# Optimization experiments

Hardware: AMD Instinct MI355X
Metric: run time of the kernel (lower is better)

## Reference

```python
import jax, jax.numpy as jnp
import numpy as np

B, S, E, H = 2, 2048, 768, 12
HD = E // H
EPS = 1e-5


def setup_inputs() -> dict:
    key = jax.random.key(0)
    ks = jax.random.split(key, 7)
    sc_in = 1.0 / np.sqrt(E)
    return {
        "x": jax.random.normal(ks[0], (B, S, E), dtype=jnp.float32),
        "gamma": jnp.ones((E,), dtype=jnp.float32),
        "beta": jnp.zeros((E,), dtype=jnp.float32),
        "Wqkv": jax.random.normal(ks[1], (3 * E, E), dtype=jnp.float32) * sc_in,
        "bqkv": jax.random.normal(ks[2], (3 * E,), dtype=jnp.float32) * 0.01,
        "Wo": jax.random.normal(ks[3], (E, E), dtype=jnp.float32) * sc_in,
        "bo": jax.random.normal(ks[4], (E,), dtype=jnp.float32) * 0.01,
    }


def reference(x, gamma, beta, Wqkv, bqkv, Wo, bo):
    # LayerNorm
    mu = jnp.mean(x, axis=-1, keepdims=True)
    var = jnp.mean(jnp.square(x - mu), axis=-1, keepdims=True)
    xn = (x - mu) * jax.lax.rsqrt(var + EPS) * gamma + beta
    # fused QKV projection; original reshapes to [B,S,H,3*hd] then chunks,
    # i.e. per-head blocks of 3*hd split into q/k/v slices of hd each.
    qkv = (xn @ Wqkv.T + bqkv).reshape(B, S, H, 3, HD)
    q, k, v = qkv[..., 0, :], qkv[..., 1, :], qkv[..., 2, :]  # [B,S,H,hd]
    scores = jnp.einsum("bshd,bthd->bhst", q, k) / np.sqrt(HD)
    attn = jax.nn.softmax(scores, axis=-1)  # [B,H,S,S]
    out = jnp.einsum("bhst,bthd->bshd", attn, v).reshape(B, S, E)
    return out @ Wo.T + bo
```

## Files before the change

kernel.cpp:

```cpp
#include <hip/hip_runtime.h>
#include <math.h>

#define B_  2
#define S_  2048
#define E_  768
#define H_  12
#define HD_ 64
#define M_  (B_ * S_)
#define N3E (3 * E_)

typedef __attribute__((ext_vector_type(8)))  short short8;
typedef __attribute__((ext_vector_type(4)))  short short4v;
typedef __attribute__((ext_vector_type(8)))  _Float16 half8;
typedef __attribute__((ext_vector_type(4)))  _Float16 half4;
typedef __attribute__((ext_vector_type(2)))  _Float16 half2_t;
typedef __attribute__((ext_vector_type(4)))  float floatx4;
typedef __attribute__((ext_vector_type(16))) float floatx16;

#define QSCALE 0.18033688011112042f

__device__ inline unsigned short f2bf(float f) {
  union { float f; unsigned u; } a; a.f = f;
  unsigned r = a.u + 0x7fff + ((a.u >> 16) & 1);
  return (unsigned short)(r >> 16);
}
__device__ inline unsigned short f2bf_fast(float f) {
  union { float f; unsigned u; } a; a.f = f;
  return (unsigned short)((a.u + 0x8000u) >> 16);
}
__device__ inline half2_t pkrtz(float a, float b) {
  return __builtin_bit_cast(half2_t, __builtin_amdgcn_cvt_pkrtz(a, b));
}

__global__ __launch_bounds__(256) void cvt2_kernel(
    const float* __restrict__ w1, const float* __restrict__ w2,
    unsigned short* __restrict__ d1, unsigned short* __restrict__ d2,
    int n1_4, int ntot4) {
  int i = blockIdx.x * 256 + threadIdx.x;
  if (i >= ntot4) return;
  const float* src; unsigned short* dst; int k;
  if (i < n1_4) { src = w1; dst = d1; k = i; }
  else          { src = w2; dst = d2; k = i - n1_4; }
  float4 f = *(const float4*)&src[k * 4];
  ushort4 r;
  r.x = f2bf(f.x); r.y = f2bf(f.y); r.z = f2bf(f.z); r.w = f2bf(f.w);
  *(ushort4*)&dst[k * 4] = r;
}

__global__ __launch_bounds__(256) void ln_kernel(
    const float* __restrict__ x, const float* __restrict__ gamma,
    const float* __restrict__ beta, unsigned short* __restrict__ xnb) {
  const int wv = threadIdx.x >> 6, lane = threadIdx.x & 63;
  const int row = blockIdx.x * 4 + wv;
  const float* xr = x + (size_t)row * E_;

  float4 a = ((const float4*)xr)[lane];
  float4 b = ((const float4*)xr)[lane + 64];
  float4 c = ((const float4*)xr)[lane + 128];

  float s  = (a.x + a.y) + (a.z + a.w) + (b.x + b.y) + (b.z + b.w)
           + (c.x + c.y) + (c.z + c.w);
  float s2 = a.x*a.x + a.y*a.y + a.z*a.z + a.w*a.w
           + b.x*b.x + b.y*b.y + b.z*b.z + b.w*b.w
           + c.x*c.x + c.y*c.y + c.z*c.z + c.w*c.w;
#pragma unroll
  for (int o = 32; o > 0; o >>= 1) {
    s  += __shfl_xor(s, o);
    s2 += __shfl_xor(s2, o);
  }
  const float mu  = s * (1.0f / E_);
  const float var = s2 * (1.0f / E_) - mu * mu;
  const float rs  = rsqrtf(var + 1e-5f);

  const float4* gp = (const float4*)gamma;
  const float4* bp = (const float4*)beta;
  ushort4* xo = (ushort4*)(xnb + (size_t)row * E_);

  float4 vin[3] = {a, b, c};
#pragma unroll
  for (int j = 0; j < 3; j++) {
    float4 g = gp[lane + 64 * j];
    float4 be = bp[lane + 64 * j];
    float4 v = vin[j];
    ushort4 r;
    r.x = f2bf((v.x - mu) * rs * g.x + be.x);
    r.y = f2bf((v.y - mu) * rs * g.y + be.y);
    r.z = f2bf((v.z - mu) * rs * g.z + be.z);
    r.w = f2bf((v.w - mu) * rs * g.w + be.w);
    xo[lane + 64 * j] = r;
  }
}

__global__ __launch_bounds__(256) void bgemm_kernel(
    const unsigned short* __restrict__ A, const unsigned short* __restrict__ Wb,
    const float* __restrict__ bias, int mode,
    unsigned short* __restrict__ qbf, unsigned short* __restrict__ kbf,
    _Float16* __restrict__ vth, float* __restrict__ out) {
  __shared__ __align__(16) unsigned short As[128 * 64];
  __shared__ __align__(16) unsigned short Bs[64 * 64];

  const int t  = threadIdx.x;
  const int ln = t & 63, wv = t >> 6;
  const int lr = ln & 15, lg = ln >> 4;
  const int m0 = blockIdx.x * 128, n0 = blockIdx.y * 64;
  const int w  = (mode == 1) ? 3 : ((n0 >> 6) % 3);

  const int srow = ln >> 3;
  const int scol = (ln & 7) * 8;

  const unsigned short* Ag = A  + (size_t)(m0 + wv * 32 + srow) * 768 + scol;
  const unsigned short* Bg = Wb + (size_t)(n0 + wv * 16 + srow) * 768 + scol;

  floatx4 acc[2][4];
#pragma unroll
  for (int i = 0; i < 2; i++)
#pragma unroll
    for (int j = 0; j < 4; j++) acc[i][j] = (floatx4){0.f, 0.f, 0.f, 0.f};

  for (int k0 = 0; k0 < 768; k0 += 64) {
    __syncthreads();
#pragma unroll
    for (int j = 0; j < 4; j++)
      __builtin_amdgcn_global_load_lds(
          (const __attribute__((address_space(1))) void*)(Ag + k0 + j * 8 * 768),
          (__attribute__((address_space(3))) void*)(&As[(wv * 32 + j * 8) * 64]),
          16, 0, 0);
#pragma unroll
    for (int j = 0; j < 2; j++)
      __builtin_amdgcn_global_load_lds(
          (const __attribute__((address_space(1))) void*)(Bg + k0 + j * 8 * 768),
          (__attribute__((address_space(3))) void*)(&Bs[(wv * 16 + j * 8) * 64]),
          16, 0, 0);
    __syncthreads();

#pragma unroll
    for (int kk = 0; kk < 2; kk++) {
      short8 af[2], bf[4];
#pragma unroll
      for (int i = 0; i < 2; i++)
        af[i] = *(const short8*)&As[(wv * 32 + i * 16 + lr) * 64 + kk * 32 + lg * 8];
#pragma unroll
      for (int j = 0; j < 4; j++)
        bf[j] = *(const short8*)&Bs[(j * 16 + lr) * 64 + kk * 32 + lg * 8];
      if (w < 2) {
#pragma unroll
        for (int i = 0; i < 2; i++)
#pragma unroll
          for (int j = 0; j < 4; j++)
            acc[i][j] = __builtin_amdgcn_mfma_f32_16x16x32_bf16(bf[j], af[i], acc[i][j], 0, 0, 0);
      } else {
#pragma unroll
        for (int i = 0; i < 2; i++)
#pragma unroll
          for (int j = 0; j < 4; j++)
            acc[i][j] = __builtin_amdgcn_mfma_f32_16x16x32_bf16(af[i], bf[j], acc[i][j], 0, 0, 0);
      }
    }
  }

  if (mode == 1) {
#pragma unroll
    for (int i = 0; i < 2; i++) {
      const int grow0 = m0 + wv * 32 + i * 16 + lg * 4;
#pragma unroll
      for (int j = 0; j < 4; j++) {
        const int gcol = n0 + j * 16 + lr;
        const float bb = bias[gcol];
#pragma unroll
        for (int r = 0; r < 4; r++)
          out[(size_t)(grow0 + r) * E_ + gcol] = acc[i][j][r] + bb;
      }
    }
  } else if (w < 2) {
    const int h = n0 / 192;
    const int bh = (m0 >> 11) * H_ + h;
    unsigned short* dst = (w == 0) ? qbf : kbf;
    const float sc = (w == 0) ? QSCALE : 1.0f;
#pragma unroll
    for (int i = 0; i < 2; i++) {
      const int s = (m0 & 2047) + wv * 32 + i * 16 + lr;
      const size_t rowb = (size_t)bh * 131072 + (size_t)(s >> 5) * 2048 + (s & 31) * 4;
#pragma unroll
      for (int j = 0; j < 4; j++) {
        float4 b4 = *(const float4*)&bias[n0 + j * 16 + lg * 4];
        ushort4 r;
        r.x = f2bf_fast((acc[i][j][0] + b4.x) * sc);
        r.y = f2bf_fast((acc[i][j][1] + b4.y) * sc);
        r.z = f2bf_fast((acc[i][j][2] + b4.z) * sc);
        r.w = f2bf_fast((acc[i][j][3] + b4.w) * sc);
        *(ushort4*)&dst[rowb + (size_t)(j * 4 + lg) * 128] = r;
      }
    }
  } else {
    const int h = n0 / 192;
    const int bh = (m0 >> 11) * H_ + h;
#pragma unroll
    for (int i = 0; i < 2; i++) {
      const int s0 = (m0 & 2047) + wv * 32 + i * 16 + lg * 4;
      const int tb = s0 >> 6, kh = (s0 >> 5) & 1;
      const int kc2 = (s0 >> 4) & 1, l5v = (s0 >> 3) & 1, e0 = s0 & 7;
#pragma unroll
      for (int j = 0; j < 4; j++) {
        const int d = j * 16 + lr;
        const int db = d >> 5, l31v = d & 31;
        const float bb = bias[n0 + d];
        half2_t h01 = pkrtz(acc[i][j][0] + bb, acc[i][j][1] + bb);
        half2_t h23 = pkrtz(acc[i][j][2] + bb, acc[i][j][3] + bb);
        half4 hv = __builtin_shufflevector(h01, h23, 0, 1, 2, 3);
        const size_t idx =
            ((((((size_t)bh * 32 + tb) * 2 + kh) * 2 + db) * 2 + kc2) * 2 + l5v) * 256
            + (size_t)l31v * 8 + e0;
        *(half4*)&vth[idx] = hv;
      }
    }
  }
}

#define PROW 40

__global__ __launch_bounds__(256, 4) void attn_kernel(
    const unsigned short* __restrict__ qb, const unsigned short* __restrict__ kb,
    const _Float16* __restrict__ vth, unsigned short* __restrict__ ao) {
  __shared__ __align__(16) unsigned char smem[26112];
  _Float16* Ps = (_Float16*)smem;
  float* C1 = (float*)smem;
  float* C2 = C1 + 3 * 64 * 17;

  const int t = threadIdx.x;
  const int lane = t & 63, wv = t >> 6;
  const int l31 = lane & 31, l5 = lane >> 5;

  const int id = blockIdx.x;
  const int bh = (id & 7) * 3 + ((id >> 3) >> 6);
  const int qt = (id >> 3) & 63;
  const int b = bh / H_, h = bh % H_;
  const int q0 = qt * 32;

  short8 qf[4];
  {
    const unsigned short* qp = qb + (size_t)bh * 131072 + (size_t)qt * 2048 + l31 * 4;
#pragma unroll
    for (int kc = 0; kc < 4; kc++) {
      short4v a = *(const short4v*)(qp + (kc * 4 + l5 * 2) * 128);
      short4v b2 = *(const short4v*)(qp + (kc * 4 + l5 * 2) * 128 + 128);
      qf[kc] = __builtin_shufflevector(a, b2, 0, 1, 2, 3, 4, 5, 6, 7);
    }
  }

  floatx16 oacc0 = (floatx16)0.0f;
  floatx16 oacc1 = (floatx16)0.0f;
  float lsum = 0.f;

  const unsigned short* kpb =
      kb + (size_t)bh * 131072 + (size_t)(2 * (wv >> 1) + (wv & 1)) * 2048 + l31 * 4;
  const _Float16* vpb =
      vth + (size_t)(bh * 32 + (wv >> 1)) * 4096 + (size_t)(wv & 1) * 2048 + (size_t)lane * 8;
  _Float16* PsW = Ps + wv * 32 * PROW;

#define LDK(kfv, tb2)                                                          \
  {                                                                            \
    const unsigned short* _p = kpb + (size_t)(tb2) * 8192;                     \
    _Pragma("unroll")                                                          \
    for (int kc = 0; kc < 4; kc++) {                                           \
      short4v _a = *(const short4v*)(_p + (kc * 4 + l5 * 2) * 128);            \
      short4v _b = *(const short4v*)(_p + (kc * 4 + l5 * 2) * 128 + 128);      \
      kfv[kc] = __builtin_shufflevector(_a, _b, 0, 1, 2, 3, 4, 5, 6, 7);       \
    }                                                                          \
  }

  short8 kf[4];
  half8 vf[4];
  LDK(kf, 0);
  floatx16 sacc = (floatx16)0.0f;
#pragma unroll
  for (int kc = 0; kc < 4; kc++)
    sacc = __builtin_amdgcn_mfma_f32_32x32x16_bf16(kf[kc], qf[kc], sacc, 0, 0, 0);
  LDK(kf, 1);
#pragma unroll
  for (int j = 0; j < 4; j++) vf[j] = *(const half8*)(vpb + j * 512);

  for (int tb = 0; tb < 16; tb++) {
#pragma unroll
    for (int r = 0; r < 16; r++) sacc[r] = exp2f(sacc[r]);
    {
      float s01 = (sacc[0] + sacc[1]) + (sacc[2] + sacc[3]);
      float s23 = (sacc[4] + sacc[5]) + (sacc[6] + sacc[7]);
      float s45 = (sacc[8] + sacc[9]) + (sacc[10] + sacc[11]);
      float s67 = (sacc[12] + sacc[13]) + (sacc[14] + sacc[15]);
      lsum += (s01 + s23) + (s45 + s67);
    }
#pragma unroll
    for (int rq = 0; rq < 4; rq++) {
      half2_t a = pkrtz(sacc[rq * 4 + 0], sacc[rq * 4 + 1]);
      half2_t c = pkrtz(sacc[rq * 4 + 2], sacc[rq * 4 + 3]);
      half4 w = __builtin_shufflevector(a, c, 0, 1, 2, 3);
      *(half4*)&PsW[l31 * PROW + rq * 8 + l5 * 4] = w;
    }
    const _Float16* prd = &PsW[l31 * PROW + l5 * 8];
    half8 pf0 = *(const half8*)(prd);
    half8 pf1 = *(const half8*)(prd + 16);

    oacc0 = __builtin_amdgcn_mfma_f32_32x32x16_f16(vf[0], pf0, oacc0, 0, 0, 0);
    oacc0 = __builtin_amdgcn_mfma_f32_32x32x16_f16(vf[1], pf1, oacc0, 0, 0, 0);
    oacc1 = __builtin_amdgcn_mfma_f32_32x32x16_f16(vf[2], pf0, oacc1, 0, 0, 0);
    oacc1 = __builtin_amdgcn_mfma_f32_32x32x16_f16(vf[3], pf1, oacc1, 0, 0, 0);

    if (tb != 15) {
      const _Float16* vt2 = vpb + (size_t)(tb + 1) * 8192;
#pragma unroll
      for (int j = 0; j < 4; j++) vf[j] = *(const half8*)(vt2 + j * 512);
      sacc = (floatx16)0.0f;
#pragma unroll
      for (int kc = 0; kc < 4; kc++)
        sacc = __builtin_amdgcn_mfma_f32_32x32x16_bf16(kf[kc], qf[kc], sacc, 0, 0, 0);
      LDK(kf, (tb + 2) & 15);
    }
  }

  const float l2 = lsum + __shfl_xor(lsum, 32);

  __syncthreads();
  if (wv > 0) {
    float* c = &C1[(size_t)((wv - 1) * 64 + lane) * 17];
#pragma unroll
    for (int j = 0; j < 16; j++) c[j] = oacc0[j];
    c[16] = l2;
  }
  if (wv != 1) {
    const int slot = (wv == 0) ? 0 : wv - 1;
    float* c = &C2[(size_t)(slot * 64 + lane) * 17];
#pragma unroll
    for (int j = 0; j < 16; j++) c[j] = oacc1[j];
    c[16] = l2;
  }
  __syncthreads();
  if (wv < 2) {
    float o[16];
    float L;
    if (wv == 0) {
      L = l2;
#pragma unroll
      for (int j = 0; j < 16; j++) o[j] = oacc0[j];
#pragma unroll
      for (int i = 0; i < 3; i++) {
        const float* c = &C1[(size_t)(i * 64 + lane) * 17];
#pragma unroll
        for (int j = 0; j < 16; j++) o[j] += c[j];
        L += c[16];
      }
    } else {
      L = l2;
#pragma unroll
      for (int j = 0; j < 16; j++) o[j] = oacc1[j];
#pragma unroll
      for (int i = 0; i < 3; i++) {
        const float* c = &C2[(size_t)(i * 64 + lane) * 17];
#pragma unroll
        for (int j = 0; j < 16; j++) o[j] += c[j];
        L += c[16];
      }
    }
    const float inv = 1.0f / L;
    const int row = q0 + l31;
    const int dbase = wv * 32;
    unsigned short* arow = &ao[((size_t)(b * S_ + row)) * E_ + h * HD_ + dbase];
#pragma unroll
    for (int a = 0; a < 4; a++) {
      ushort4 s;
      s.x = f2bf(o[a * 4 + 0] * inv);
      s.y = f2bf(o[a * 4 + 1] * inv);
      s.z = f2bf(o[a * 4 + 2] * inv);
      s.w = f2bf(o[a * 4 + 3] * inv);
      *(ushort4*)&arow[8 * a + 4 * l5] = s;
    }
  }
}

extern "C" void kernel_launch(void* const* d_in, const int* in_sizes, int n_in,
                              void* d_out, int out_size, void* d_ws, size_t ws_size,
                              hipStream_t stream) {
  const float* x     = (const float*)d_in[0];
  const float* gamma = (const float*)d_in[1];
  const float* beta  = (const float*)d_in[2];
  const float* Wqkv  = (const float*)d_in[3];
  const float* bqkv  = (const float*)d_in[4];
  const float* Wo    = (const float*)d_in[5];
  const float* bo    = (const float*)d_in[6];
  float* out = (float*)d_out;

  const size_t SZ = (size_t)M_ * E_;
  unsigned short* xnb = (unsigned short*)d_ws;
  unsigned short* qbf = xnb + SZ;
  unsigned short* kbf = qbf + SZ;
  _Float16*       vth = (_Float16*)(kbf + SZ);
  unsigned short* aob = (unsigned short*)(vth + SZ);
  unsigned short* wqb = aob + SZ;
  unsigned short* wob = wqb + (size_t)N3E * E_;

  const int nq4 = (N3E * E_) / 4;
  const int no4 = (E_ * E_) / 4;
  const int ntot4 = nq4 + no4;
  cvt2_kernel<<<(ntot4 + 255) / 256, 256, 0, stream>>>(Wqkv, Wo, wqb, wob, nq4, ntot4);

  ln_kernel<<<M_ / 4, 256, 0, stream>>>(x, gamma, beta, xnb);

  dim3 g_qkv(M_ / 128, N3E / 64);
  bgemm_kernel<<<g_qkv, 256, 0, stream>>>(xnb, wqb, bqkv, 0, qbf, kbf, vth, nullptr);

  attn_kernel<<<1536, 256, 0, stream>>>(qbf, kbf, vth, aob);

  dim3 g_out(M_ / 128, E_ / 64);
  bgemm_kernel<<<g_out, 256, 0, stream>>>(aob, wob, bo, 1, nullptr, nullptr, nullptr, out);
}
```

Baseline: 175.1 us.

## Pre-swizzle bf16 weights into MFMA fragment order and merge LN with conversion

Measured after the change: 177.4 us. About the same (+1.3%).

```diff
diff --git a/kernel.cpp b/kernel.cpp
--- a/kernel.cpp
+++ b/kernel.cpp
@@ -19,6 +19,10 @@
 
 #define QSCALE 0.18033688011112042f
 
+#define WTILE 6144
+#define NPQ   (36 * WTILE)
+#define NPO   (12 * WTILE)
+
 __device__ inline unsigned short f2bf(float f) {
   union { float f; unsigned u; } a; a.f = f;
   unsigned r = a.u + 0x7fff + ((a.u >> 16) & 1);
@@ -32,136 +36,142 @@
   return __builtin_bit_cast(half2_t, __builtin_amdgcn_cvt_pkrtz(a, b));
 }
 
-__global__ __launch_bounds__(256) void cvt2_kernel(
-    const float* __restrict__ w1, const float* __restrict__ w2,
-    unsigned short* __restrict__ d1, unsigned short* __restrict__ d2,
-    int n1_4, int ntot4) {
-  int i = blockIdx.x * 256 + threadIdx.x;
-  if (i >= ntot4) return;
-  const float* src; unsigned short* dst; int k;
-  if (i < n1_4) { src = w1; dst = d1; k = i; }
-  else          { src = w2; dst = d2; k = i - n1_4; }
-  float4 f = *(const float4*)&src[k * 4];
-  ushort4 r;
-  r.x = f2bf(f.x); r.y = f2bf(f.y); r.z = f2bf(f.z); r.w = f2bf(f.w);
-  *(ushort4*)&dst[k * 4] = r;
-}
-
-__global__ __launch_bounds__(256) void ln_kernel(
+__global__ __launch_bounds__(256) void aux_kernel(
     const float* __restrict__ x, const float* __restrict__ gamma,
-    const float* __restrict__ beta, unsigned short* __restrict__ xnb) {
-  const int wv = threadIdx.x >> 6, lane = threadIdx.x & 63;
-  const int row = blockIdx.x * 4 + wv;
-  const float* xr = x + (size_t)row * E_;
-
-  float4 a = ((const float4*)xr)[lane];
-  float4 b = ((const float4*)xr)[lane + 64];
-  float4 c = ((const float4*)xr)[lane + 128];
-
-  float s  = (a.x + a.y) + (a.z + a.w) + (b.x + b.y) + (b.z + b.w)
-           + (c.x + c.y) + (c.z + c.w);
-  float s2 = a.x*a.x + a.y*a.y + a.z*a.z + a.w*a.w
-           + b.x*b.x + b.y*b.y + b.z*b.z + b.w*b.w
-           + c.x*c.x + c.y*c.y + c.z*c.z + c.w*c.w;
-#pragma unroll
-  for (int o = 32; o > 0; o >>= 1) {
-    s  += __shfl_xor(s, o);
-    s2 += __shfl_xor(s2, o);
-  }
-  const float mu  = s * (1.0f / E_);
-  const float var = s2 * (1.0f / E_) - mu * mu;
-  const float rs  = rsqrtf(var + 1e-5f);
-
-  const float4* gp = (const float4*)gamma;
-  const float4* bp = (const float4*)beta;
-  ushort4* xo = (ushort4*)(xnb + (size_t)row * E_);
-
-  float4 vin[3] = {a, b, c};
-#pragma unroll
-  for (int j = 0; j < 3; j++) {
-    float4 g = gp[lane + 64 * j];
-    float4 be = bp[lane + 64 * j];
-    float4 v = vin[j];
-    ushort4 r;
-    r.x = f2bf((v.x - mu) * rs * g.x + be.x);
-    r.y = f2bf((v.y - mu) * rs * g.y + be.y);
-    r.z = f2bf((v.z - mu) * rs * g.z + be.z);
-    r.w = f2bf((v.w - mu) * rs * g.w + be.w);
-    xo[lane + 64 * j] = r;
-  }
-}
-
+    const float* __restrict__ beta, unsigned short* __restrict__ xnb,
+    const float* __restrict__ Wqkv, const float* __restrict__ Wo,
+    unsigned short* __restrict__ wqf, unsigned short* __restrict__ wof) {
+  const int bid = blockIdx.x;
+  if (bid < M_ / 4) {
+    const int wv = threadIdx.x >> 6, lane = threadIdx.x & 63;
+    const int row = bid * 4 + wv;
+    const float* xr = x + (size_t)row * E_;
+
+    float4 a = ((const float4*)xr)[lane];
+    float4 b = ((const float4*)xr)[lane + 64];
+    float4 c = ((const float4*)xr)[lane + 128];
+
+    float s  = (a.x + a.y) + (a.z + a.w) + (b.x + b.y) + (b.z + b.w)
+             + (c.x + c.y) + (c.z + c.w);
+    float s2 = a.x*a.x + a.y*a.y + a.z*a.z + a.w*a.w
+             + b.x*b.x + b.y*b.y + b.z*b.z + b.w*b.w
+             + c.x*c.x + c.y*c.y + c.z*c.z + c.w*c.w;
+#pragma unroll
+    for (int o = 32; o > 0; o >>= 1) {
+      s  += __shfl_xor(s, o);
+      s2 += __shfl_xor(s2, o);
+    }
+    const float mu  = s * (1.0f / E_);
+    const float var = s2 * (1.0f / E_) - mu * mu;
+    const float rs  = rsqrtf(var + 1e-5f);
+
+    const float4* gp = (const float4*)gamma;
+    const float4* bp = (const float4*)beta;
+    ushort4* xo = (ushort4*)(xnb + (size_t)row * E_);
+
+    float4 vin[3] = {a, b, c};
+#pragma unroll
+    for (int j = 0; j < 3; j++) {
+      float4 g = gp[lane + 64 * j];
+      float4 be = bp[lane + 64 * j];
+      float4 v = vin[j];
+      ushort4 r;
+      r.x = f2bf((v.x - mu) * rs * g.x + be.x);
+      r.y = f2bf((v.y - mu) * rs * g.y + be.y);
+      r.z = f2bf((v.z - mu) * rs * g.z + be.z);
+      r.w = f2bf((v.w - mu) * rs * g.w + be.w);
+      xo[lane + 64 * j] = r;
+    }
+  } else {
+    int p = (bid - M_ / 4) * 256 + threadIdx.x;
+    const float* src; unsigned short* dst;
+    if (p < NPQ) { src = Wqkv; dst = wqf; }
+    else         { src = Wo;   dst = wof; p -= NPQ; }
+    const int nt = p / WTILE, r = p % WTILE;
+    const int kb = r >> 9, r2 = r & 511;
+    const int kk = r2 >> 8, r3 = r2 & 255;
+    const int j = r3 >> 6, lane = r3 & 63;
+    const int row = nt * 64 + j * 16 + (lane & 15);
+    const int col = kb * 64 + kk * 32 + (lane >> 4) * 8;
+    const float* sp = src + (size_t)row * 768 + col;
+    float4 f0 = *(const float4*)(sp);
+    float4 f1 = *(const float4*)(sp + 4);
+    unsigned short* dp = dst + (size_t)p * 8;
+    ushort4 r0, r1;
+    r0.x = f2bf(f0.x); r0.y = f2bf(f0.y); r0.z = f2bf(f0.z); r0.w = f2bf(f0.w);
+    r1.x = f2bf(f1.x); r1.y = f2bf(f1.y); r1.z = f2bf(f1.z); r1.w = f2bf(f1.w);
+    *(ushort4*)(dp)     = r0;
+    *(ushort4*)(dp + 4) = r1;
+  }
+}
+
+template <int NI>
 __global__ __launch_bounds__(256) void bgemm_kernel(
-    const unsigned short* __restrict__ A, const unsigned short* __restrict__ Wb,
+    const unsigned short* __restrict__ A, const unsigned short* __restrict__ Wf,
     const float* __restrict__ bias, int mode,
     unsigned short* __restrict__ qbf, unsigned short* __restrict__ kbf,
     _Float16* __restrict__ vth, float* __restrict__ out) {
-  __shared__ __align__(16) unsigned short As[128 * 64];
-  __shared__ __align__(16) unsigned short Bs[64 * 64];
+  constexpr int BM = 64 * NI;
+  __shared__ __align__(16) unsigned short As[BM * 64];
 
   const int t  = threadIdx.x;
   const int ln = t & 63, wv = t >> 6;
   const int lr = ln & 15, lg = ln >> 4;
-  const int m0 = blockIdx.x * 128, n0 = blockIdx.y * 64;
-  const int w  = (mode == 1) ? 3 : ((n0 >> 6) % 3);
+  const int m0 = blockIdx.x * BM, n0 = blockIdx.y * 64;
+  const int w  = (mode == 1) ? 3 : (blockIdx.y % 3);
 
   const int srow = ln >> 3;
   const int scol = (ln & 7) * 8;
 
-  const unsigned short* Ag = A  + (size_t)(m0 + wv * 32 + srow) * 768 + scol;
-  const unsigned short* Bg = Wb + (size_t)(n0 + wv * 16 + srow) * 768 + scol;
-
-  floatx4 acc[2][4];
-#pragma unroll
-  for (int i = 0; i < 2; i++)
+  const unsigned short* Ag = A + (size_t)(m0 + wv * (BM / 4) + srow) * 768 + scol;
+  const unsigned short* Wt = Wf + (size_t)blockIdx.y * (WTILE * 8);
+
+  floatx4 acc[NI][4];
+#pragma unroll
+  for (int i = 0; i < NI; i++)
 #pragma unroll
     for (int j = 0; j < 4; j++) acc[i][j] = (floatx4){0.f, 0.f, 0.f, 0.f};
 
-  for (int k0 = 0; k0 < 768; k0 += 64) {
+  for (int kb = 0; kb < 12; kb++) {
     __syncthreads();
 #pragma unroll
-    for (int j = 0; j < 4; j++)
+    for (int j = 0; j < BM / 32; j++)
       __builtin_amdgcn_global_load_lds(
-          (const __attribute__((address_space(1))) void*)(Ag + k0 + j * 8 * 768),
-          (__attribute__((address_space(3))) void*)(&As[(wv * 32 + j * 8) * 64]),
+          (const __attribute__((address_space(1))) void*)(Ag + kb * 64 + j * 8 * 768),
+          (__attribute__((address_space(3))) void*)(&As[(wv * (BM / 4) + j * 8) * 64]),
           16, 0, 0);
-#pragma unroll
-    for (int j = 0; j < 2; j++)
-      __builtin_amdgcn_global_load_lds(
-          (const __attribute__((address_space(1))) void*)(Bg + k0 + j * 8 * 768),
-          (__attribute__((address_space(3))) void*)(&Bs[(wv * 16 + j * 8) * 64]),
-          16, 0, 0);
+    short8 bfr[8];
+#pragma unroll
+    for (int u = 0; u < 8; u++)
+      bfr[u] = *(const short8*)&Wt[(size_t)kb * 4096 + u * 512 + ln * 8];
     __syncthreads();
 
 #pragma unroll
     for (int kk = 0; kk < 2; kk++) {
-      short8 af[2], bf[4];
-#pragma unroll
-      for (int i = 0; i < 2; i++)
-        af[i] = *(const short8*)&As[(wv * 32 + i * 16 + lr) * 64 + kk * 32 + lg * 8];
-#pragma unroll
-      for (int j = 0; j < 4; j++)
-        bf[j] = *(const short8*)&Bs[(j * 16 + lr) * 64 + kk * 32 + lg * 8];
+      short8 af[NI];
+#pragma unroll
+      for (int i = 0; i < NI; i++)
+        af[i] = *(const short8*)&As[(wv * (BM / 4) + i * 16 + lr) * 64 + kk * 32 + lg * 8];
       if (w < 2) {
 #pragma unroll
-        for (int i = 0; i < 2; i++)
+        for (int i = 0; i < NI; i++)
 #pragma unroll
           for (int j = 0; j < 4; j++)
-            acc[i][j] = __builtin_amdgcn_mfma_f32_16x16x32_bf16(bf[j], af[i], acc[i][j], 0, 0, 0);
+            acc[i][j] = __builtin_amdgcn_mfma_f32_16x16x32_bf16(bfr[kk * 4 + j], af[i], acc[i][j], 0, 0, 0);
       } else {
 #pragma unroll
-        for (int i = 0; i < 2; i++)
+        for (int i = 0; i < NI; i++)
 #pragma unroll
           for (int j = 0; j < 4; j++)
-            acc[i][j] = __builtin_amdgcn_mfma_f32_16x16x32_bf16(af[i], bf[j], acc[i][j], 0, 0, 0);
+            acc[i][j] = __builtin_amdgcn_mfma_f32_16x16x32_bf16(af[i], bfr[kk * 4 + j], acc[i][j], 0, 0, 0);
       }
     }
   }
 
   if (mode == 1) {
 #pragma unroll
-    for (int i = 0; i < 2; i++) {
-      const int grow0 = m0 + wv * 32 + i * 16 + lg * 4;
+    for (int i = 0; i < NI; i++) {
+      const int grow0 = m0 + wv * (BM / 4) + i * 16 + lg * 4;
 #pragma unroll
       for (int j = 0; j < 4; j++) {
         const int gcol = n0 + j * 16 + lr;
@@ -177,8 +187,8 @@
     unsigned short* dst = (w == 0) ? qbf : kbf;
     const float sc = (w == 0) ? QSCALE : 1.0f;
 #pragma unroll
-    for (int i = 0; i < 2; i++) {
-      const int s = (m0 & 2047) + wv * 32 + i * 16 + lr;
+    for (int i = 0; i < NI; i++) {
+      const int s = (m0 & 2047) + wv * (BM / 4) + i * 16 + lr;
       const size_t rowb = (size_t)bh * 131072 + (size_t)(s >> 5) * 2048 + (s & 31) * 4;
 #pragma unroll
       for (int j = 0; j < 4; j++) {
@@ -195,8 +205,8 @@
     const int h = n0 / 192;
     const int bh = (m0 >> 11) * H_ + h;
 #pragma unroll
-    for (int i = 0; i < 2; i++) {
-      const int s0 = (m0 & 2047) + wv * 32 + i * 16 + lg * 4;
+    for (int i = 0; i < NI; i++) {
+      const int s0 = (m0 & 2047) + wv * (BM / 4) + i * 16 + lg * 4;
       const int tb = s0 >> 6, kh = (s0 >> 5) & 1;
       const int kc2 = (s0 >> 4) & 1, l5v = (s0 >> 3) & 1, e0 = s0 & 7;
 #pragma unroll
@@ -394,21 +404,18 @@
   unsigned short* kbf = qbf + SZ;
   _Float16*       vth = (_Float16*)(kbf + SZ);
   unsigned short* aob = (unsigned short*)(vth + SZ);
-  unsigned short* wqb = aob + SZ;
-  unsigned short* wob = wqb + (size_t)N3E * E_;
-
-  const int nq4 = (N3E * E_) / 4;
-  const int no4 = (E_ * E_) / 4;
-  const int ntot4 = nq4 + no4;
-  cvt2_kernel<<<(ntot4 + 255) / 256, 256, 0, stream>>>(Wqkv, Wo, wqb, wob, nq4, ntot4);
-
-  ln_kernel<<<M_ / 4, 256, 0, stream>>>(x, gamma, beta, xnb);
+  unsigned short* wqf = aob + SZ;
+  unsigned short* wof = wqf + (size_t)N3E * E_;
+
+  const int cvblocks = (NPQ + NPO) / 256;
+  aux_kernel<<<M_ / 4 + cvblocks, 256, 0, stream>>>(
+      x, gamma, beta, xnb, Wqkv, Wo, wqf, wof);
 
   dim3 g_qkv(M_ / 128, N3E / 64);
-  bgemm_kernel<<<g_qkv, 256, 0, stream>>>(xnb, wqb, bqkv, 0, qbf, kbf, vth, nullptr);
+  bgemm_kernel<2><<<g_qkv, 256, 0, stream>>>(xnb, wqf, bqkv, 0, qbf, kbf, vth, nullptr);
 
   attn_kernel<<<1536, 256, 0, stream>>>(qbf, kbf, vth, aob);
 
-  dim3 g_out(M_ / 128, E_ / 64);
-  bgemm_kernel<<<g_out, 256, 0, stream>>>(aob, wob, bo, 1, nullptr, nullptr, nullptr, out);
-}
+  dim3 g_out(M_ / 64, E_ / 64);
+  bgemm_kernel<1><<<g_out, 256, 0, stream>>>(aob, wof, bo, 1, nullptr, nullptr, nullptr, out);
+}
```
